# Kernel tuning notes

Hardware: AMD Instinct MI355X
Metric: run time of the kernel (lower is better)

## Reference

```python
import jax, jax.numpy as jnp
import numpy as np

CH = 512
GROUPS = 8
EPS = 1e-5


def setup_inputs() -> dict:
    key = jax.random.key(0)
    ks = jax.random.split(key, 5)
    B, C, H, W = 16, CH, 32, 32
    x = jax.random.normal(ks[0], (B, C, H, W), dtype=jnp.float32)
    # GroupNorm affine params
    norm_w = jnp.ones((C,), dtype=jnp.float32)
    norm_b = jnp.zeros((C,), dtype=jnp.float32)
    # 1x1 conv == linear over channels; store weights as [out, in]
    qkv_w = jax.random.normal(ks[1], (3 * C, C), dtype=jnp.float32) * (C ** -0.5)
    qkv_b = jnp.zeros((3 * C,), dtype=jnp.float32)
    proj_w = jax.random.normal(ks[2], (C, C), dtype=jnp.float32) * (C ** -0.5)
    proj_b = jnp.zeros((C,), dtype=jnp.float32)
    return {"x": x, "norm_w": norm_w, "norm_b": norm_b,
            "qkv_w": qkv_w, "qkv_b": qkv_b,
            "proj_w": proj_w, "proj_b": proj_b}


def _group_norm(x, w, b):
    B, C, H, W = x.shape
    g = GROUPS
    xg = x.reshape(B, g, C // g, H * W)
    mean = xg.mean(axis=(2, 3), keepdims=True)
    var = xg.var(axis=(2, 3), keepdims=True)
    xn = (xg - mean) * jax.lax.rsqrt(var + EPS)
    xn = xn.reshape(B, C, H, W)
    return xn * w[None, :, None, None] + b[None, :, None, None]


def reference(x, norm_w, norm_b, qkv_w, qkv_b, proj_w, proj_b):
    B, C, H, W = x.shape
    h = _group_norm(x, norm_w, norm_b)  # [B,C,H,W]
    hs = h.reshape(B, C, H * W)  # spatial tokens along last axis
    # 1x1 conv QKV: [3C,C] @ [B,C,N] -> [B,3C,N]
    qkv = jnp.einsum('oc,bcn->bon', qkv_w, hs) + qkv_b[None, :, None]
    q, k, v = jnp.split(qkv, 3, axis=1)  # each [B,C,N]
    scale = C ** (-0.5)
    attn = jnp.einsum('bci,bcj->bij', q, k) * scale  # [B,N,N]
    attn = jax.nn.softmax(attn, axis=-1)
    out = jnp.einsum('bij,bcj->bci', attn, v)  # [B,C,N]
    out = jnp.einsum('oc,bcn->bon', proj_w, out) + proj_b[None, :, None]
    return x + out.reshape(B, C, H, W)
```

## Files before the change

kernel.cpp:

```cpp
#include <hip/hip_runtime.h>
#include <math.h>

#define Bn   16
#define Cn   512
#define Nn   1024
#define Gn   8
#define CPG  64
#define EPSf 1e-5f

typedef short           bf16x8 __attribute__((ext_vector_type(8)));
typedef float           f32x4  __attribute__((ext_vector_type(4)));
typedef unsigned short  u16;
typedef unsigned short  u16x4  __attribute__((ext_vector_type(4)));
typedef unsigned short  u16x8  __attribute__((ext_vector_type(8)));

#define TS 136

__device__ __forceinline__ u16 f2b(float f) {
  union { float f; unsigned u; } c; c.f = f;
  unsigned r = (c.u + 0x7FFFu + ((c.u >> 16) & 1u)) >> 16;
  return (u16)r;
}

__device__ __forceinline__ void g2l16(const void* g, void* l) {
  __builtin_amdgcn_global_load_lds(
      (const __attribute__((address_space(1))) unsigned int*)g,
      (__attribute__((address_space(3))) unsigned int*)l, 16, 0, 0);
}

__device__ __forceinline__ void barrier_asm() {
  asm volatile("s_barrier" ::: "memory");
}

__device__ __forceinline__ void gemm_core(u16* As, u16* Bs,
    const u16* __restrict__ A, size_t sA,
    const u16* __restrict__ B, size_t sB, int K, f32x4 acc[4][4]) {
  const int t = threadIdx.x;
  const int w = t >> 6, l = t & 63, quad = l >> 4, lr = l & 15;
  const int wm = (w >> 1) * 64, wn = (w & 1) * 64;

  const int ra = w * 16 + (l >> 2);
  const int p  = l & 3;
  const int q  = p ^ ((ra >> 1) & 3);
  const u16* gA0 = A + (size_t)ra * sA + q * 8;
  const u16* gA1 = A + (size_t)(ra + 64) * sA + q * 8;
  const u16* gB0 = B + (size_t)ra * sB + q * 8;
  const u16* gB1 = B + (size_t)(ra + 64) * sB + q * 8;
  u16* lA0 = As + ra * 32 + p * 8;
  u16* lA1 = As + (ra + 64) * 32 + p * 8;
  u16* lB0 = Bs + ra * 32 + p * 8;
  u16* lB1 = Bs + (ra + 64) * 32 + p * 8;

  for (int k0 = 0; k0 < K; k0 += 32) {
    __syncthreads();
    g2l16(gA0 + k0, lA0);
    g2l16(gA1 + k0, lA1);
    g2l16(gB0 + k0, lB0);
    g2l16(gB1 + k0, lB1);
    __syncthreads();
    bf16x8 af[4], bfr[4];
    #pragma unroll
    for (int fm = 0; fm < 4; fm++) {
      int r = wm + fm * 16 + lr;
      af[fm] = *(const bf16x8*)&As[r * 32 + ((quad ^ ((r >> 1) & 3)) << 3)];
    }
    #pragma unroll
    for (int fn = 0; fn < 4; fn++) {
      int r = wn + fn * 16 + lr;
      bfr[fn] = *(const bf16x8*)&Bs[r * 32 + ((quad ^ ((r >> 1) & 3)) << 3)];
    }
    #pragma unroll
    for (int fm = 0; fm < 4; fm++)
      #pragma unroll
      for (int fn = 0; fn < 4; fn++)
        acc[fm][fn] = __builtin_amdgcn_mfma_f32_16x16x32_bf16(
            af[fm], bfr[fn], acc[fm][fn], 0, 0, 0);
  }
}

#define GEMM_PRE()                                              \
  const int t = threadIdx.x;                                    \
  const int w = t >> 6, l = t & 63, quad = l >> 4, lr = l & 15; \
  const int wm = (w >> 1) * 64, wn = (w & 1) * 64;              \
  (void)w; (void)wm; (void)wn; (void)l;                         \
  f32x4 acc[4][4];                                              \
  { f32x4 z = {0.f, 0.f, 0.f, 0.f};                             \
    for (int i_ = 0; i_ < 4; i_++)                              \
      for (int j_ = 0; j_ < 4; j_++) acc[i_][j_] = z; }

#define SLOT 12288

__device__ __forceinline__ void core256(const u16* __restrict__ A, size_t sA,
    const u16* __restrict__ B, size_t sB, int K, u16* SH, f32x4 acc[8][4],
    int wm, int wn, int quad, int lr) {
  const int t = threadIdx.x, wv = t >> 6, l = t & 63;
  const int srow = l >> 2;
  const int sch  = ((l & 3) ^ ((l >> 3) & 3)) * 8;

  const u16* gA[4]; int lA[4];
  const u16* gB[2]; int lB[2];
  #pragma unroll
  for (int c = 0; c < 4; c++) {
    gA[c] = A + (size_t)(wv * 64 + c * 16 + srow) * sA + sch;
    lA[c] = wv * 2048 + c * 512 + l * 8;
  }
  #pragma unroll
  for (int c = 0; c < 2; c++) {
    gB[c] = B + (size_t)(wv * 32 + c * 16 + srow) * sB + sch;
    lB[c] = 8192 + wv * 1024 + c * 512 + l * 8;
  }

  u16 *sc = SH, *sn = SH + SLOT, *sf = SH + 2 * SLOT;
  const int nt = K >> 5;
  #pragma unroll
  for (int c = 0; c < 4; c++) g2l16(gA[c], sc + lA[c]);
  #pragma unroll
  for (int c = 0; c < 2; c++) g2l16(gB[c], sc + lB[c]);
  if (nt > 1) {
    #pragma unroll
    for (int c = 0; c < 4; c++) g2l16(gA[c] + 32, sn + lA[c]);
    #pragma unroll
    for (int c = 0; c < 2; c++) g2l16(gB[c] + 32, sn + lB[c]);
  }

  const int rch = (quad ^ ((lr >> 1) & 3)) * 8;
  int aoff[8], boff[4];
  #pragma unroll
  for (int fm = 0; fm < 8; fm++) aoff[fm] = (wm + fm * 16 + lr) * 32 + rch;
  #pragma unroll
  for (int fn = 0; fn < 4; fn++) boff[fn] = 8192 + (wn + fn * 16 + lr) * 32 + rch;

  for (int tt = 0; tt < nt; tt++) {
    if (tt + 1 < nt) {
      asm volatile("s_waitcnt vmcnt(6)" ::: "memory");
    } else {
      asm volatile("s_waitcnt vmcnt(0)" ::: "memory");
    }
    barrier_asm();
    if (tt + 2 < nt) {
      const int k0 = (tt + 2) * 32;
      #pragma unroll
      for (int c = 0; c < 4; c++) g2l16(gA[c] + k0, sf + lA[c]);
      #pragma unroll
      for (int c = 0; c < 2; c++) g2l16(gB[c] + k0, sf + lB[c]);
    }
    bf16x8 af[8], bfr[4];
    #pragma unroll
    for (int fm = 0; fm < 8; fm++) af[fm] = *(const bf16x8*)&sc[aoff[fm]];
    #pragma unroll
    for (int fn = 0; fn < 4; fn++) bfr[fn] = *(const bf16x8*)&sc[boff[fn]];
    __builtin_amdgcn_s_setprio(1);
    #pragma unroll
    for (int fm = 0; fm < 8; fm++)
      #pragma unroll
      for (int fn = 0; fn < 4; fn++)
        acc[fm][fn] = __builtin_amdgcn_mfma_f32_16x16x32_bf16(
            af[fm], bfr[fn], acc[fm][fn], 0, 0, 0);
    __builtin_amdgcn_s_setprio(0);
    u16* tmp = sc; sc = sn; sn = sf; sf = tmp;
  }
}

#define CORE256_PRE()                                             \
  const int t = threadIdx.x;                                      \
  const int w = t >> 6, l = t & 63, quad = l >> 4, lr = l & 15;   \
  const int wm = (w >> 1) * 128, wn = (w & 1) * 64;               \
  (void)l;                                                        \
  f32x4 acc[8][4];                                                \
  { f32x4 z = {0.f, 0.f, 0.f, 0.f};                               \
    _Pragma("unroll")                                             \
    for (int i_ = 0; i_ < 8; i_++)                                \
      _Pragma("unroll")                                           \
      for (int j_ = 0; j_ < 4; j_++) acc[i_][j_] = z; }

#define SLOT128 8192

__device__ __forceinline__ void core128(const u16* __restrict__ A, size_t sA,
    const u16* __restrict__ B, size_t sB, int K, u16* SH, f32x4 acc[4][4],
    int wm, int wn, int quad, int lr) {
  const int t = threadIdx.x;
  const int w = t >> 6, l = t & 63;
  const int ra = w * 16 + (l >> 2);
  const int p  = l & 3;
  const int q  = p ^ ((ra >> 1) & 3);
  const u16* gA0 = A + (size_t)ra * sA + q * 8;
  const u16* gA1 = A + (size_t)(ra + 64) * sA + q * 8;
  const u16* gB0 = B + (size_t)ra * sB + q * 8;
  const u16* gB1 = B + (size_t)(ra + 64) * sB + q * 8;
  const int lA0 = ra * 32 + p * 8;
  const int lA1 = (ra + 64) * 32 + p * 8;
  const int lB0 = 4096 + ra * 32 + p * 8;
  const int lB1 = 4096 + (ra + 64) * 32 + p * 8;

  const int nt = K >> 5;
  {
    u16* s0 = SH;
    g2l16(gA0, s0 + lA0); g2l16(gA1, s0 + lA1);
    g2l16(gB0, s0 + lB0); g2l16(gB1, s0 + lB1);
    if (nt > 1) {
      u16* s1 = SH + SLOT128;
      g2l16(gA0 + 32, s1 + lA0); g2l16(gA1 + 32, s1 + lA1);
      g2l16(gB0 + 32, s1 + lB0); g2l16(gB1 + 32, s1 + lB1);
    }
  }
  const int rch = (quad ^ ((lr >> 1) & 3)) * 8;
  int aoff[4], boff[4];
  #pragma unroll
  for (int fm = 0; fm < 4; fm++) aoff[fm] = (wm + fm * 16 + lr) * 32 + rch;
  #pragma unroll
  for (int fn = 0; fn < 4; fn++) boff[fn] = 4096 + (wn + fn * 16 + lr) * 32 + rch;

  for (int tt = 0; tt < nt; tt++) {
    u16* sc = SH + (tt & 3) * SLOT128;
    if (tt + 2 < nt) {
      u16* sn = SH + ((tt + 2) & 3) * SLOT128;
      const int k0 = (tt + 2) * 32;
      g2l16(gA0 + k0, sn + lA0); g2l16(gA1 + k0, sn + lA1);
      g2l16(gB0 + k0, sn + lB0); g2l16(gB1 + k0, sn + lB1);
      asm volatile("s_waitcnt vmcnt(8)" ::: "memory");
    } else if (tt + 1 < nt) {
      asm volatile("s_waitcnt vmcnt(4)" ::: "memory");
    } else {
      asm volatile("s_waitcnt vmcnt(0)" ::: "memory");
    }
    barrier_asm();
    bf16x8 af[4], bfr[4];
    #pragma unroll
    for (int fm = 0; fm < 4; fm++) af[fm] = *(const bf16x8*)&sc[aoff[fm]];
    #pragma unroll
    for (int fn = 0; fn < 4; fn++) bfr[fn] = *(const bf16x8*)&sc[boff[fn]];
    __builtin_amdgcn_s_setprio(1);
    #pragma unroll
    for (int fm = 0; fm < 4; fm++)
      #pragma unroll
      for (int fn = 0; fn < 4; fn++)
        acc[fm][fn] = __builtin_amdgcn_mfma_f32_16x16x32_bf16(
            af[fm], bfr[fn], acc[fm][fn], 0, 0, 0);
    __builtin_amdgcn_s_setprio(0);
  }
}

__global__ __launch_bounds__(256) void prep_k(const float* __restrict__ qkv_w,
    const float* __restrict__ proj_w, const float* __restrict__ qkv_b,
    const float* __restrict__ x, u16* __restrict__ wqk16,
    u16* __restrict__ wvT16, u16* __restrict__ pw16,
    float* __restrict__ bias2, float* __restrict__ stats) {
  __shared__ u16 T[64][68];
  __shared__ float redf[8];
  int bid = blockIdx.x, t = threadIdx.x;
  if (bid < 512) {
    int i = bid * 256 + t;
    float4 v = ((const float4*)qkv_w)[i];
    u16x4 o;
    o.x = f2b(v.x); o.y = f2b(v.y); o.z = f2b(v.z); o.w = f2b(v.w);
    ((u16x4*)wqk16)[i] = o;
  } else if (bid < 576) {
    int tile = bid - 512, tx = tile & 7, ty = tile >> 3;
    int row = t >> 4, col4 = t & 15;
    #pragma unroll
    for (int it = 0; it < 4; it++) {
      int cc = row + it * 16;
      float4 v = *(const float4*)&qkv_w[(size_t)(1024 + ty * 64 + cc) * 512 + tx * 64 + col4 * 4];
      u16x4 o;
      o.x = f2b(v.x); o.y = f2b(v.y); o.z = f2b(v.z); o.w = f2b(v.w);
      *(u16x4*)&T[cc][col4 * 4] = o;
    }
    __syncthreads();
    #pragma unroll
    for (int it = 0; it < 2; it++) {
      int ch = t + it * 256;
      int d = ch >> 3, c8 = (ch & 7) * 8;
      u16x8 o;
      #pragma unroll
      for (int j = 0; j < 8; j++) o[j] = T[c8 + j][d];
      *(u16x8*)&wvT16[(size_t)(tx * 64 + d) * 512 + ty * 64 + c8] = o;
    }
  } else if (bid < 578) {
    int m = (bid - 576) * 256 + t;
    float s = 0.f;
    for (int c = 0; c < 512; c++)
      s += proj_w[(size_t)m * 512 + c] * qkv_b[1024 + c];
    bias2[m] = s;
  } else if (bid < 1090) {
    int idx = bid - 578, bg = idx >> 2, part = idx & 3;
    const float4* xp = (const float4*)x + (size_t)bg * 16384 + part * 4096;
    float s = 0.f, ss = 0.f;
    for (int i = t; i < 4096; i += 256) {
      float4 v = xp[i];
      s  += v.x + v.y + v.z + v.w;
      ss += v.x * v.x + v.y * v.y + v.z * v.z + v.w * v.w;
    }
    #pragma unroll
    for (int off = 32; off > 0; off >>= 1) {
      s  += __shfl_down(s, off);
      ss += __shfl_down(ss, off);
    }
    int lane = t & 63, wid = t >> 6;
    if (lane == 0) { redf[wid] = s; redf[4 + wid] = ss; }
    __syncthreads();
    if (t == 0) {
      atomicAdd(&stats[bg],       redf[0] + redf[1] + redf[2] + redf[3]);
      atomicAdd(&stats[128 + bg], redf[4] + redf[5] + redf[6] + redf[7]);
    }
  } else {
    int i = (bid - 1090) * 256 + t;
    float4 v = ((const float4*)proj_w)[i];
    u16x4 o;
    o.x = f2b(v.x); o.y = f2b(v.y); o.z = f2b(v.z); o.w = f2b(v.w);
    ((u16x4*)pw16)[i] = o;
  }
}

__global__ __launch_bounds__(256) void gnw2_k(const float* __restrict__ x,
    const float* __restrict__ stats, const float* __restrict__ nw,
    const float* __restrict__ nb, const u16* __restrict__ pw16,
    const u16* __restrict__ wvT16, u16* __restrict__ W2, u16* __restrict__ hT) {
  __shared__ u16 AsBs[8192];
  int bid = blockIdx.x;
  if (bid < 16) {
    int m0 = (bid >> 2) * 128, d0 = (bid & 3) * 128;
    GEMM_PRE();
    gemm_core(AsBs, AsBs + 4096, pw16 + (size_t)m0 * 512, 512,
              wvT16 + (size_t)d0 * 512, 512, 512, acc);
    #pragma unroll
    for (int fm = 0; fm < 4; fm++) {
      int m = m0 + wm + fm * 16 + quad * 4;
      #pragma unroll
      for (int fn = 0; fn < 4; fn++) {
        int d = d0 + wn + fn * 16 + lr;
        f32x4 a = acc[fm][fn];
        W2[(size_t)(m    ) * 512 + d] = f2b(a[0]);
        W2[(size_t)(m + 1) * 512 + d] = f2b(a[1]);
        W2[(size_t)(m + 2) * 512 + d] = f2b(a[2]);
        W2[(size_t)(m + 3) * 512 + d] = f2b(a[3]);
      }
    }
    return;
  }
  int u = bid - 16;
  int b = u >> 7, rem = u & 127, c0 = (rem >> 4) * 64, n0 = (rem & 15) * 64;
  u16 (*T)[68] = (u16(*)[68])AsBs;
  int t = threadIdx.x;
  int row = t >> 4, col4 = t & 15;
  const float inv = 1.0f / 65536.0f;
  #pragma unroll
  for (int it = 0; it < 4; it++) {
    int cc = row + it * 16;
    int c  = c0 + cc;
    int bg = b * Gn + (c >> 6);
    float mean = stats[bg] * inv;
    float var  = stats[128 + bg] * inv - mean * mean;
    float rstd = rsqrtf(var + EPSf);
    float a  = nw[c] * rstd;
    float bb = nb[c] - mean * a;
    float4 xv = *(const float4*)&x[((size_t)(b * Cn + c)) * Nn + n0 + col4 * 4];
    u16x4 o;
    o.x = f2b(xv.x * a + bb); o.y = f2b(xv.y * a + bb);
    o.z = f2b(xv.z * a + bb); o.w = f2b(xv.w * a + bb);
    *(u16x4*)&T[cc][col4 * 4] = o;
  }
  __syncthreads();
  #pragma unroll
  for (int it = 0; it < 2; it++) {
    int ch = t + it * 256;
    int n  = ch >> 3, c8 = (ch & 7) * 8;
    u16x8 o;
    #pragma unroll
    for (int j = 0; j < 8; j++) o[j] = T[c8 + j][n];
    *(u16x8*)&hT[((size_t)(b * Nn + n0 + n)) * 512 + c0 + c8] = o;
  }
}

__global__ __launch_bounds__(256, 2) void qkvp_k(const u16* __restrict__ wqk16,
    const u16* __restrict__ W2, const u16* __restrict__ hT,
    const float* __restrict__ qkv_b, u16* __restrict__ qkT,
    u16* __restrict__ VP) {
  __shared__ __align__(16) u16 SH[3 * SLOT];
  int u = blockIdx.x;
  CORE256_PRE();

  if (u < 512) {
    int b = u >> 5, rem = u & 31, m0 = (rem >> 3) * 256, n0 = (rem & 7) * 128;
    core256(wqk16 + (size_t)m0 * 512, 512,
            hT + (size_t)(b * Nn + n0) * 512, 512, 512, SH, acc, wm, wn, quad, lr);
    float4 bss[8];
    #pragma unroll
    for (int fm = 0; fm < 8; fm++)
      bss[fm] = *(const float4*)&qkv_b[m0 + wm + fm * 16 + quad * 4];
    u16* T = SH;
    const int hsel = wn >> 6;
    #pragma unroll
    for (int h = 0; h < 2; h++) {
      barrier_asm();
      if (hsel == h) {
        #pragma unroll
        for (int fm = 0; fm < 8; fm++) {
          int mc = wm + fm * 16 + quad * 4;
          #pragma unroll
          for (int fn = 0; fn < 4; fn++) {
            int nl = fn * 16 + lr;
            f32x4 a = acc[fm][fn];
            u16x4 pk;
            pk.x = f2b(a[0] + bss[fm].x); pk.y = f2b(a[1] + bss[fm].y);
            pk.z = f2b(a[2] + bss[fm].z); pk.w = f2b(a[3] + bss[fm].w);
            *(u16x4*)&T[nl * 264 + mc] = pk;
          }
        }
      }
      barrier_asm();
      #pragma unroll
      for (int kk = 0; kk < 8; kk++) {
        int idx = t + 256 * kk, row = idx >> 5, grp = idx & 31;
        u16x8 v = *(u16x8*)&T[row * 264 + grp * 8];
        *(u16x8*)&qkT[((size_t)(b * Nn + n0 + h * 64 + row)) * 1024 + m0 + grp * 8] = v;
      }
    }
  } else {
    int u2 = u - 512;
    int b = u2 >> 4, rem = u2 & 15, m0 = (rem >> 3) * 256, j0 = (rem & 7) * 128;
    core256(W2 + (size_t)m0 * 512, 512,
            hT + (size_t)(b * Nn + j0) * 512, 512, 512, SH, acc, wm, wn, quad, lr);
    u16* T = SH;
    const int hsel = wm >> 7;
    #pragma unroll
    for (int h = 0; h < 2; h++) {
      barrier_asm();
      if (hsel == h) {
        #pragma unroll
        for (int fm = 0; fm < 8; fm++) {
          int ml = fm * 16 + quad * 4;
          #pragma unroll
          for (int fn = 0; fn < 4; fn++) {
            int jl = wn + fn * 16 + lr;
            f32x4 a = acc[fm][fn];
            T[(ml    ) * TS + jl] = f2b(a[0]);
            T[(ml + 1) * TS + jl] = f2b(a[1]);
            T[(ml + 2) * TS + jl] = f2b(a[2]);
            T[(ml + 3) * TS + jl] = f2b(a[3]);
          }
        }
      }
      barrier_asm();
      #pragma unroll
      for (int kk = 0; kk < 8; kk++) {
        int idx = t + 256 * kk, row = idx >> 4, grp = idx & 15;
        u16x8 v = *(u16x8*)&T[row * TS + grp * 8];
        *(u16x8*)&VP[((size_t)(b * 512 + m0 + h * 128 + row)) * 1024 + j0 + grp * 8] = v;
      }
    }
  }
}

__global__ __launch_bounds__(256, 2) void qkexp_k(const u16* __restrict__ qkT,
    u16* __restrict__ Pm, float* __restrict__ rpart) {
  __shared__ __align__(16) u16 SH[3 * SLOT];
  __shared__ float psum[256];
  int u = blockIdx.x;
  int b = u >> 5, rem = u & 31, i0 = (rem >> 3) * 256, j0 = (rem & 7) * 128;
  const u16* base = qkT + (size_t)b * Nn * 1024;
  CORE256_PRE();
  core256(base + (size_t)i0 * 1024, 1024,
          base + (size_t)j0 * 1024 + 512, 1024, 512, SH, acc, wm, wn, quad, lr);
  psum[t] = 0.f;
  const float scale = 0.04419417382415922f;
  u16* T = SH;
  const int hsel = wm >> 7;
  #pragma unroll
  for (int h = 0; h < 2; h++) {
    barrier_asm();
    if (hsel == h) {
      #pragma unroll
      for (int fm = 0; fm < 8; fm++) {
        int il = fm * 16 + quad * 4;
        float rs0 = 0.f, rs1 = 0.f, rs2 = 0.f, rs3 = 0.f;
        #pragma unroll
        for (int fn = 0; fn < 4; fn++) {
          int jl = wn + fn * 16 + lr;
          f32x4 a = acc[fm][fn];
          float e0 = __expf(a[0] * scale);
          float e1 = __expf(a[1] * scale);
          float e2 = __expf(a[2] * scale);
          float e3 = __expf(a[3] * scale);
          rs0 += e0; rs1 += e1; rs2 += e2; rs3 += e3;
          T[(il    ) * TS + jl] = f2b(e0);
          T[(il + 1) * TS + jl] = f2b(e1);
          T[(il + 2) * TS + jl] = f2b(e2);
          T[(il + 3) * TS + jl] = f2b(e3);
        }
        #pragma unroll
        for (int mask = 1; mask < 16; mask <<= 1) {
          rs0 += __shfl_xor(rs0, mask);
          rs1 += __shfl_xor(rs1, mask);
          rs2 += __shfl_xor(rs2, mask);
          rs3 += __shfl_xor(rs3, mask);
        }
        if (lr == 0) {
          int ri = h * 128 + il;
          atomicAdd(&psum[ri],     rs0);
          atomicAdd(&psum[ri + 1], rs1);
          atomicAdd(&psum[ri + 2], rs2);
          atomicAdd(&psum[ri + 3], rs3);
        }
      }
    }
    barrier_asm();
    #pragma unroll
    for (int kk = 0; kk < 8; kk++) {
      int idx = t + 256 * kk, row = idx >> 4, grp = idx & 15;
      u16x8 v = *(u16x8*)&T[row * TS + grp * 8];
      *(u16x8*)&Pm[((size_t)(b * Nn + i0 + h * 128 + row)) * 1024 + j0 + grp * 8] = v;
    }
  }
  __syncthreads();
  rpart[((size_t)(b * 8) + (rem & 7)) * 1024 + i0 + t] = psum[t];
}

__global__ __launch_bounds__(256, 2) void pvout_k(const u16* __restrict__ VP,
    const u16* __restrict__ Pm, const float* __restrict__ rpart,
    const float* __restrict__ bias2, const float* __restrict__ proj_b,
    const float* __restrict__ x, float* __restrict__ out) {
  __shared__ __align__(16) u16 SH[4 * SLOT128];
  __shared__ float rinv[128];
  int bid = blockIdx.x;
  int u = (bid & 7) * 64 + (bid >> 3);
  int b = u >> 5, rem = u & 31, m0 = (rem >> 3) * 128, i0 = (rem & 7) * 128;
  if (threadIdx.x < 128) {
    float s = 0.f;
    #pragma unroll
    for (int jb = 0; jb < 8; jb++)
      s += rpart[((size_t)(b * 8 + jb)) * 1024 + i0 + threadIdx.x];
    rinv[threadIdx.x] = 1.0f / s;
  }
  GEMM_PRE();
  core128(VP + ((size_t)(b * 512 + m0)) * 1024, 1024,
          Pm + ((size_t)(b * Nn + i0)) * 1024, 1024, 1024, SH, acc, wm, wn, quad, lr);
  __syncthreads();
  #pragma unroll
  for (int fm = 0; fm < 4; fm++) {
    int m = m0 + wm + fm * 16 + quad * 4;
    float c0 = bias2[m    ] + proj_b[m    ];
    float c1 = bias2[m + 1] + proj_b[m + 1];
    float c2 = bias2[m + 2] + proj_b[m + 2];
    float c3 = bias2[m + 3] + proj_b[m + 3];
    #pragma unroll
    for (int fn = 0; fn < 4; fn++) {
      int il = wn + fn * 16 + lr;
      int i  = i0 + il;
      float ri = rinv[il];
      f32x4 a = acc[fm][fn];
      size_t o0 = ((size_t)(b * Cn + m)) * Nn + i;
      out[o0                  ] = a[0] * ri + c0 + x[o0                  ];
      out[o0 + Nn             ] = a[1] * ri + c1 + x[o0 + Nn             ];
      out[o0 + 2 * Nn         ] = a[2] * ri + c2 + x[o0 + 2 * Nn         ];
      out[o0 + 3 * (size_t)Nn] = a[3] * ri + c3 + x[o0 + 3 * (size_t)Nn];
    }
  }
}

extern "C" void kernel_launch(void* const* d_in, const int* in_sizes, int n_in,
                              void* d_out, int out_size, void* d_ws, size_t ws_size,
                              hipStream_t stream) {
  const float* x      = (const float*)d_in[0];
  const float* norm_w = (const float*)d_in[1];
  const float* norm_b = (const float*)d_in[2];
  const float* qkv_w  = (const float*)d_in[3];
  const float* qkv_b  = (const float*)d_in[4];
  const float* proj_w = (const float*)d_in[5];
  const float* proj_b = (const float*)d_in[6];
  float* out = (float*)d_out;
  char* ws = (char*)d_ws;

  u16*   wqk16 = (u16*)(ws);
  u16*   wvT16 = (u16*)(ws + 1048576);
  u16*   pw16  = (u16*)(ws + 1572864);
  u16*   W2    = (u16*)(ws + 2097152);
  float* bias2 = (float*)(ws + 2621440);
  float* stats = (float*)(ws + 2623488);
  u16*   hT    = (u16*)(ws + 2624512);
  u16*   qkT   = (u16*)(ws + 19401728);
  u16*   VP    = (u16*)(ws + 52956160);
  u16*   Pm    = (u16*)(ws + 69733376);
  float* rpart = (float*)(ws + 103287808);

  hipMemsetAsync(stats, 0, 1024, stream);
  prep_k<<<1346, 256, 0, stream>>>(qkv_w, proj_w, qkv_b, x, wqk16, wvT16,
                                   pw16, bias2, stats);
  gnw2_k<<<2064, 256, 0, stream>>>(x, stats, norm_w, norm_b, pw16, wvT16,
                                   W2, hT);
  qkvp_k<<<768, 256, 0, stream>>>(wqk16, W2, hT, qkv_b, qkT, VP);
  qkexp_k<<<512, 256, 0, stream>>>(qkT, Pm, rpart);
  pvout_k<<<512, 256, 0, stream>>>(VP, Pm, rpart, bias2, proj_b, x, out);
}
```

Baseline: 218.6 us.

## Split GEMM k-step into two phases and remap blocks across XCDs

The core GEMM loop now runs each k-tile in two halves. Each half issues part of the next-tile global-to-LDS prefetches, loads half the A fragments and runs its MFMAs, with a barrier and a sched_barrier between the halves. This interleaves memory issue with compute and lowers the number of live A-fragment registers. Block indices in the qkvp and qkexp kernels are also remapped so that consecutive tiles of one batch land on the same XCD, for better L2 locality. The extra barrier per k-step adds synchronisation cost, and the remap assumes the grid sizes are 768 and 512 blocks.

```diff
diff --git a/kernel.cpp b/kernel.cpp
--- a/kernel.cpp
+++ b/kernel.cpp
@@ -136,27 +136,46 @@
     } else {
       asm volatile("s_waitcnt vmcnt(0)" ::: "memory");
     }
+    const int k0 = (tt + 2) * 32;
+    const bool pf = (tt + 2 < nt);
     barrier_asm();
-    if (tt + 2 < nt) {
-      const int k0 = (tt + 2) * 32;
-      #pragma unroll
-      for (int c = 0; c < 4; c++) g2l16(gA[c] + k0, sf + lA[c]);
-      #pragma unroll
-      for (int c = 0; c < 2; c++) g2l16(gB[c] + k0, sf + lB[c]);
-    }
-    bf16x8 af[8], bfr[4];
-    #pragma unroll
-    for (int fm = 0; fm < 8; fm++) af[fm] = *(const bf16x8*)&sc[aoff[fm]];
+    if (pf) {
+      g2l16(gA[0] + k0, sf + lA[0]);
+      g2l16(gA[1] + k0, sf + lA[1]);
+      g2l16(gA[2] + k0, sf + lA[2]);
+    }
+    bf16x8 af0[4], bfr[4];
+    #pragma unroll
+    for (int fm = 0; fm < 4; fm++) af0[fm] = *(const bf16x8*)&sc[aoff[fm]];
     #pragma unroll
     for (int fn = 0; fn < 4; fn++) bfr[fn] = *(const bf16x8*)&sc[boff[fn]];
     __builtin_amdgcn_s_setprio(1);
     #pragma unroll
-    for (int fm = 0; fm < 8; fm++)
+    for (int fm = 0; fm < 4; fm++)
       #pragma unroll
       for (int fn = 0; fn < 4; fn++)
         acc[fm][fn] = __builtin_amdgcn_mfma_f32_16x16x32_bf16(
-            af[fm], bfr[fn], acc[fm][fn], 0, 0, 0);
+            af0[fm], bfr[fn], acc[fm][fn], 0, 0, 0);
     __builtin_amdgcn_s_setprio(0);
+    __builtin_amdgcn_sched_barrier(0);
+    barrier_asm();
+    if (pf) {
+      g2l16(gA[3] + k0, sf + lA[3]);
+      g2l16(gB[0] + k0, sf + lB[0]);
+      g2l16(gB[1] + k0, sf + lB[1]);
+    }
+    bf16x8 af1[4];
+    #pragma unroll
+    for (int fm = 0; fm < 4; fm++) af1[fm] = *(const bf16x8*)&sc[aoff[fm + 4]];
+    __builtin_amdgcn_s_setprio(1);
+    #pragma unroll
+    for (int fm = 0; fm < 4; fm++)
+      #pragma unroll
+      for (int fn = 0; fn < 4; fn++)
+        acc[fm + 4][fn] = __builtin_amdgcn_mfma_f32_16x16x32_bf16(
+            af1[fm], bfr[fn], acc[fm + 4][fn], 0, 0, 0);
+    __builtin_amdgcn_s_setprio(0);
+    __builtin_amdgcn_sched_barrier(0);
     u16* tmp = sc; sc = sn; sn = sf; sf = tmp;
   }
 }
@@ -376,7 +395,8 @@
     const float* __restrict__ qkv_b, u16* __restrict__ qkT,
     u16* __restrict__ VP) {
   __shared__ __align__(16) u16 SH[3 * SLOT];
-  int u = blockIdx.x;
+  int bid = blockIdx.x;
+  int u = (bid & 7) * 96 + (bid >> 3);
   CORE256_PRE();
 
   if (u < 512) {
@@ -455,7 +475,8 @@
     u16* __restrict__ Pm, float* __restrict__ rpart) {
   __shared__ __align__(16) u16 SH[3 * SLOT];
   __shared__ float psum[256];
-  int u = blockIdx.x;
+  int bid = blockIdx.x;
+  int u = (bid & 7) * 64 + (bid >> 3);
   int b = u >> 5, rem = u & 31, i0 = (rem >> 3) * 256, j0 = (rem & 7) * 128;
   const u16* base = qkT + (size_t)b * Nn * 1024;
   CORE256_PRE();
```

Result: faster. 212.4 us (median of 2 runs) (-2.8%).
